# Performance work log

Hardware: AMD Instinct MI355X
Metric: run time of the kernel (lower is better)

## Reference

```python
import jax, jax.numpy as jnp
import numpy as np

N, E, C, K, M = 16384, 512, 128, 2048, 4
H1, H2 = 128, 256
EPS = 1e-5


def setup_inputs() -> dict:
    key = jax.random.key(0)
    ks = jax.random.split(key, 32)
    r = lambda k, shape, s=0.02: jax.random.normal(k, shape, dtype=jnp.float32) * s
    inp = {
        'x': jax.random.normal(ks[0], (N, E), dtype=jnp.float32),
        # per-book encoder params, stacked over M
        'enc_W1': r(ks[1], (M, E, H1)), 'enc_b1': r(ks[2], (M, H1)),
        'bn1_g': 1.0 + r(ks[3], (M, H1)), 'bn1_b': r(ks[4], (M, H1)),
        'bn1_m': r(ks[5], (M, H1), 0.1), 'bn1_v': jnp.ones((M, H1), jnp.float32),
        'enc_W2': r(ks[6], (M, H1, H2)), 'enc_b2': r(ks[7], (M, H2)),
        'bn2_g': 1.0 + r(ks[8], (M, H2)), 'bn2_b': r(ks[9], (M, H2)),
        'bn2_m': r(ks[10], (M, H2), 0.1), 'bn2_v': jnp.ones((M, H2), jnp.float32),
        'enc_W3': r(ks[11], (M, H2, C)), 'enc_b3': r(ks[12], (M, C)),
        # codebooks init uniform(-1/K, 1/K) as in torch source
        'codebooks': jax.random.uniform(ks[13], (M, K, C), jnp.float32, -1.0 / K, 1.0 / K),
        # decoder params
        'dec_W1': r(ks[14], (C, H2)), 'dec_b1': r(ks[15], (H2,)),
        'dbn1_g': 1.0 + r(ks[16], (H2,)), 'dbn1_b': r(ks[17], (H2,)),
        'dbn1_m': r(ks[18], (H2,), 0.1), 'dbn1_v': jnp.ones((H2,), jnp.float32),
        'dec_W2': r(ks[19], (H2, H1)), 'dec_b2': r(ks[20], (H1,)),
        'dbn2_g': 1.0 + r(ks[21], (H1,)), 'dbn2_b': r(ks[22], (H1,)),
        'dbn2_m': r(ks[23], (H1,), 0.1), 'dbn2_v': jnp.ones((H1,), jnp.float32),
        'dec_W3': r(ks[24], (H1, E)), 'dec_b3': r(ks[25], (E,)),
    }
    return inp


def _bn(h, g, b, m, v):
    # eval-mode BatchNorm1d with running stats (dropout inactive in eval)
    return (h - m) * (g / jnp.sqrt(v + EPS)) + b


def reference(x, enc_W1, enc_b1, bn1_g, bn1_b, bn1_m, bn1_v,
              enc_W2, enc_b2, bn2_g, bn2_b, bn2_m, bn2_v,
              enc_W3, enc_b3, codebooks,
              dec_W1, dec_b1, dbn1_g, dbn1_b, dbn1_m, dbn1_v,
              dec_W2, dec_b2, dbn2_g, dbn2_b, dbn2_m, dbn2_v,
              dec_W3, dec_b3):
    # encoders for all M books at once: [M, N, *]
    h = jnp.einsum('ne,mef->mnf', x, enc_W1) + enc_b1[:, None, :]
    h = jax.nn.relu(_bn(h, bn1_g[:, None], bn1_b[:, None], bn1_m[:, None], bn1_v[:, None]))
    h = jnp.einsum('mnf,mfg->mng', h, enc_W2) + enc_b2[:, None, :]
    h = jax.nn.relu(_bn(h, bn2_g[:, None], bn2_b[:, None], bn2_m[:, None], bn2_v[:, None]))
    ze = jnp.einsum('mng,mgc->mnc', h, enc_W3) + enc_b3[:, None, :]  # [M,N,C]

    # squared-distance VQ via dot-product expansion (same math as broadcast cdist)
    ze_sq = jnp.sum(ze * ze, axis=-1)                     # [M,N]
    cb_sq = jnp.sum(codebooks * codebooks, axis=-1)       # [M,K]
    cross = jnp.einsum('mnc,mkc->mnk', ze, codebooks)     # [M,N,K]
    dist = ze_sq[..., None] + cb_sq[:, None, :] - 2.0 * cross
    idx = jnp.argmin(dist, axis=-1)                       # [M,N]
    ce = jnp.take_along_axis(codebooks, idx[:, :, None], axis=1)  # [M,N,C]

    zq = jnp.sum(ce, axis=0)                              # [N,C]

    d = jnp.matmul(zq, dec_W1) + dec_b1
    d = jax.nn.relu(_bn(d, dbn1_g, dbn1_b, dbn1_m, dbn1_v))
    d = jnp.matmul(d, dec_W2) + dec_b2
    d = jax.nn.relu(_bn(d, dbn2_g, dbn2_b, dbn2_m, dbn2_v))
    x_hat = jnp.matmul(d, dec_W3) + dec_b3

    # res_list / ce_list returned as stacked [M,N,C] arrays
    return (x_hat, ze, ce)
```

## Files before the change

kernel.cpp:

```cpp
#include <hip/hip_runtime.h>
#include <hip/hip_bf16.h>
#include <stdint.h>

#define N_ROWS 16384
#define E_DIM 512
#define C_DIM 128
#define K_CODES 2048
#define M_BOOKS 4
#define H1_DIM 128
#define H2_DIM 256
#define EPS_V 1e-5f
#define VQ_RT 8

typedef __attribute__((ext_vector_type(8))) short short8v;
typedef __attribute__((ext_vector_type(4))) float f32x4;

#if defined(__has_builtin)
#if __has_builtin(__builtin_amdgcn_global_load_lds)
#define HAVE_GLL 1
#endif
#endif

#ifdef HAVE_GLL
__device__ __forceinline__ void gll16(const void* g, void* l) {
    __builtin_amdgcn_global_load_lds(
        (const __attribute__((address_space(1))) uint32_t*)g,
        (__attribute__((address_space(3))) uint32_t*)l, 16, 0, 0);
}
#endif

__device__ __forceinline__ unsigned int mapmono(float d) {
    unsigned int ub = __float_as_uint(d);
    return (ub & 0x80000000u) ? ~ub : (ub | 0x80000000u);
}
__device__ __forceinline__ float unmapmono(unsigned int u) {
    unsigned int bits = (u & 0x80000000u) ? (u & 0x7FFFFFFFu) : ~u;
    return __uint_as_float(bits);
}

template<int BK, bool BNRELU>
__global__ __launch_bounds__(256, 4) void gemm128(
    const float* __restrict__ A, const float* __restrict__ B,
    const float* __restrict__ bias, const float* __restrict__ bn_g,
    const float* __restrict__ bn_b, const float* __restrict__ bn_m,
    const float* __restrict__ bn_v, float* __restrict__ C,
    int Kd, int Hc, size_t sA, size_t sB, size_t sP, size_t sC)
{
    __shared__ float As[BK][128];
    __shared__ float Bs[BK][128];
    const int z = blockIdx.z;
    A += (size_t)z * sA; B += (size_t)z * sB; bias += (size_t)z * sP;
    if (BNRELU) {
        bn_g += (size_t)z * sP; bn_b += (size_t)z * sP;
        bn_m += (size_t)z * sP; bn_v += (size_t)z * sP;
    }
    const int t = threadIdx.x;
    const int tx = t & 15, ty = t >> 4;
    const int row0 = blockIdx.y * 128, col0 = blockIdx.x * 128;
    const int ar = t & 127, ak = (t >> 7) * 4;
    const int bc = (t & 31) * 4, bk0 = t >> 5;

    float acc[8][8] = {};
    for (int k0 = 0; k0 < Kd; k0 += BK) {
        #pragma unroll
        for (int l = 0; l < BK / 8; ++l) {
            const int lk = ak + l * 8;
            float4 av = *(const float4*)(A + (size_t)(row0 + ar) * Kd + (k0 + lk));
            As[lk+0][ar] = av.x; As[lk+1][ar] = av.y;
            As[lk+2][ar] = av.z; As[lk+3][ar] = av.w;
            const int kb = bk0 + l * 8;
            *(float4*)&Bs[kb][bc] =
                *(const float4*)(B + (size_t)(k0 + kb) * Hc + (col0 + bc));
        }
        __syncthreads();
        #pragma unroll
        for (int kk = 0; kk < BK; ++kk) {
            float a[8], b[8];
            *(float4*)&a[0] = *(const float4*)&As[kk][ty*4];
            *(float4*)&a[4] = *(const float4*)&As[kk][64 + ty*4];
            *(float4*)&b[0] = *(const float4*)&Bs[kk][tx*4];
            *(float4*)&b[4] = *(const float4*)&Bs[kk][64 + tx*4];
            #pragma unroll
            for (int i = 0; i < 8; ++i)
                #pragma unroll
                for (int j = 0; j < 8; ++j)
                    acc[i][j] = fmaf(a[i], b[j], acc[i][j]);
        }
        __syncthreads();
    }
    float bi[8], sc[8], mu[8], be[8];
    #pragma unroll
    for (int j = 0; j < 8; ++j) {
        const int col = col0 + ((j < 4) ? (tx*4 + j) : (64 + tx*4 + j - 4));
        bi[j] = bias[col];
        if (BNRELU) {
            sc[j] = bn_g[col] / sqrtf(bn_v[col] + EPS_V);
            mu[j] = bn_m[col]; be[j] = bn_b[col];
        }
    }
    #pragma unroll
    for (int i = 0; i < 8; ++i) {
        const int row = row0 + ((i < 4) ? (ty*4 + i) : (64 + ty*4 + i - 4));
        float v[8];
        #pragma unroll
        for (int j = 0; j < 8; ++j) {
            v[j] = acc[i][j] + bi[j];
            if (BNRELU) {
                float p = (v[j] - mu[j]) * sc[j];
                asm volatile("" : "+v"(p));
                v[j] = fmaxf(p + be[j], 0.0f);
            }
        }
        float* cp = C + (size_t)z * sC + (size_t)row * Hc + col0;
        *(float4*)(cp + tx*4)      = *(const float4*)&v[0];
        *(float4*)(cp + 64 + tx*4) = *(const float4*)&v[4];
    }
}

__global__ __launch_bounds__(256) void rowsq_np(const float* __restrict__ X,
                                                float* __restrict__ out, int rows)
{
    const int r = blockIdx.x * blockDim.x + threadIdx.x;
    if (r >= rows) return;
    const float* p = X + (size_t)r * C_DIM;
    float rr[8];
    #pragma unroll
    for (int j = 0; j < 8; ++j) {
        float v = p[j]; float s2 = v * v;
        asm volatile("" : "+v"(s2));
        rr[j] = s2;
    }
    for (int i = 8; i < C_DIM; i += 8) {
        #pragma unroll
        for (int j = 0; j < 8; ++j) {
            float v = p[i + j]; float s2 = v * v;
            asm volatile("" : "+v"(s2));
            rr[j] = rr[j] + s2;
        }
    }
    out[r] = ((rr[0]+rr[1]) + (rr[2]+rr[3])) + ((rr[4]+rr[5]) + (rr[6]+rr[7]));
}

__global__ __launch_bounds__(256) void split_ze(
    const float* __restrict__ ze, uint16_t* __restrict__ zeAf,
    float* __restrict__ zs, float* __restrict__ eps)
{
    const int m = blockIdx.y;
    const int r = blockIdx.x * 256 + threadIdx.x;
    const size_t g = (size_t)m * N_ROWS + r;
    const float* p = ze + g * C_DIM;
    float a[C_DIM];
    #pragma unroll
    for (int c4 = 0; c4 < C_DIM/4; ++c4) {
        float4 v = *(const float4*)(p + c4*4);
        a[c4*4+0]=v.x; a[c4*4+1]=v.y; a[c4*4+2]=v.z; a[c4*4+3]=v.w;
    }
    {
        float rr[8];
        #pragma unroll
        for (int j = 0; j < 8; ++j) {
            float v = a[j]; float s2 = v*v; asm volatile("" : "+v"(s2)); rr[j]=s2;
        }
        #pragma unroll
        for (int i = 8; i < C_DIM; i += 8)
            #pragma unroll
            for (int j = 0; j < 8; ++j) {
                float v = a[i+j]; float s2 = v*v; asm volatile("" : "+v"(s2));
                rr[j] = rr[j] + s2;
            }
        zs[g] = ((rr[0]+rr[1]) + (rr[2]+rr[3])) + ((rr[4]+rr[5]) + (rr[6]+rr[7]));
    }
    {
        float sab = 0.0f;
        #pragma unroll
        for (int c = 0; c < C_DIM; ++c) sab += fabsf(a[c]);
        eps[g] = sab * 4.8828125e-4f * 1e-4f + 1e-9f;
    }
    const int rt = r >> 7, rl = r & 127;
    uint16_t* base = zeAf + (size_t)m * 4194304 + ((size_t)rt * 4096 + rl) * 8;
    #pragma unroll
    for (int k8 = 0; k8 < 32; ++k8) {
        uint16_t u[8];
        #pragma unroll
        for (int j = 0; j < 8; ++j) {
            const int c = ((k8 < 16) ? k8 : (k8 - 16)) * 8 + j;
            __hip_bfloat16 h = __float2bfloat16(a[c]);
            if (k8 >= 16) {
                float res = a[c] - __bfloat162float(h);
                h = __float2bfloat16(res);
            }
            u[j] = *(uint16_t*)&h;
        }
        *(float4*)(base + (size_t)k8 * 1024) = *(const float4*)u;
    }
}

__global__ __launch_bounds__(256) void split_cb(
    const float* __restrict__ cb, uint16_t* __restrict__ cbBf,
    float* __restrict__ cbsq, int* __restrict__ count)
{
    const int m = blockIdx.z;
    const int k = blockIdx.x * 256 + threadIdx.x;
    if (m == 0 && k == 0) *count = 0;
    const float* p = cb + ((size_t)m * K_CODES + k) * C_DIM;
    float a[C_DIM];
    #pragma unroll
    for (int c4 = 0; c4 < C_DIM/4; ++c4) {
        float4 v = *(const float4*)(p + c4*4);
        a[c4*4+0]=v.x; a[c4*4+1]=v.y; a[c4*4+2]=v.z; a[c4*4+3]=v.w;
    }
    {
        float rr[8];
        #pragma unroll
        for (int j = 0; j < 8; ++j) {
            float v = a[j]; float s2 = v*v; asm volatile("" : "+v"(s2)); rr[j]=s2;
        }
        #pragma unroll
        for (int i = 8; i < C_DIM; i += 8)
            #pragma unroll
            for (int j = 0; j < 8; ++j) {
                float v = a[i+j]; float s2 = v*v; asm volatile("" : "+v"(s2));
                rr[j] = rr[j] + s2;
            }
        cbsq[(size_t)m * K_CODES + k] =
            ((rr[0]+rr[1]) + (rr[2]+rr[3])) + ((rr[4]+rr[5]) + (rr[6]+rr[7]));
    }
    const int ct = k >> 7, kl = k & 127;
    uint16_t* base = cbBf + (((size_t)m * 16 + ct) * 4096 + kl) * 8;
    #pragma unroll
    for (int k8 = 0; k8 < 32; ++k8) {
        uint16_t u[8];
        #pragma unroll
        for (int j = 0; j < 8; ++j) {
            const int c = ((k8 < 16) ? k8 : (k8 - 16)) * 8 + j;
            __hip_bfloat16 h = __float2bfloat16(a[c]);
            if (k8 >= 16) {
                float res = a[c] - __bfloat162float(h);
                h = __float2bfloat16(res);
            }
            u[j] = *(uint16_t*)&h;
        }
        *(float4*)(base + (size_t)k8 * 1024) = *(const float4*)u;
    }
}

__global__ __launch_bounds__(256, 2) void vq_mfma(
    const uint16_t* __restrict__ zeAf, const uint16_t* __restrict__ cbBf,
    const float* __restrict__ zs, const float* __restrict__ cbsq,
    unsigned long long* __restrict__ keysB, unsigned long long* __restrict__ keysS)
{
    __shared__ __align__(16) uint16_t Ball[32768];
    __shared__ unsigned long long kb2[128][2];

    const int t = threadIdx.x;
    const int l = t & 63, w = t >> 6;
    const int ct = blockIdx.y;
    const int rt0 = (blockIdx.x & 15) * VQ_RT;
    const int m = blockIdx.x >> 4;
    const int lq = l >> 4, lc = l & 15;

    const uint16_t* Bg = cbBf + ((size_t)m * 16 + ct) * 32768;
#ifdef HAVE_GLL
    #pragma unroll
    for (int i = 0; i < 16; ++i)
        gll16(Bg + (size_t)(t + i*256) * 8, Ball + (size_t)(t + i*256) * 8);
#else
    #pragma unroll
    for (int i = 0; i < 16; ++i)
        *(float4*)(Ball + (size_t)(t + i*256)*8) =
            *(const float4*)(Bg + (size_t)(t + i*256)*8);
#endif
    __syncthreads();

    const float* csb = cbsq + (size_t)m * K_CODES + ct*128;

    for (int ri = 0; ri < VQ_RT; ++ri) {
        const int rt = rt0 + ri;
        const uint16_t* Ag = zeAf + (size_t)m * 4194304 + (size_t)rt * 32768;
        f32x4 acc[2][8] = {};
        #pragma unroll
        for (int s = 0; s < 4; ++s) {
            short8v zeh[2], zel[2], cbf[8];
            #pragma unroll
            for (int rc = 0; rc < 2; ++rc) {
                const int row = w*32 + rc*16 + lc;
                zeh[rc] = *(const short8v*)(Ag + ((size_t)(s*4 + lq)*128 + row)*8);
                zel[rc] = *(const short8v*)(Ag + ((size_t)(16 + s*4 + lq)*128 + row)*8);
            }
            #pragma unroll
            for (int c8 = 0; c8 < 8; ++c8)
                cbf[c8] = *(const short8v*)(Ball + ((size_t)(s*4 + lq)*128 + c8*16 + lc)*8);
            #pragma unroll
            for (int rc = 0; rc < 2; ++rc)
                #pragma unroll
                for (int c8 = 0; c8 < 8; ++c8)
                    acc[rc][c8] = __builtin_amdgcn_mfma_f32_16x16x32_bf16(
                        cbf[c8], zeh[rc], acc[rc][c8], 0, 0, 0);
            #pragma unroll
            for (int rc = 0; rc < 2; ++rc)
                #pragma unroll
                for (int c8 = 0; c8 < 8; ++c8)
                    acc[rc][c8] = __builtin_amdgcn_mfma_f32_16x16x32_bf16(
                        cbf[c8], zel[rc], acc[rc][c8], 0, 0, 0);
            #pragma unroll
            for (int c8 = 0; c8 < 8; ++c8)
                cbf[c8] = *(const short8v*)(Ball + ((size_t)(16 + s*4 + lq)*128 + c8*16 + lc)*8);
            #pragma unroll
            for (int rc = 0; rc < 2; ++rc)
                #pragma unroll
                for (int c8 = 0; c8 < 8; ++c8)
                    acc[rc][c8] = __builtin_amdgcn_mfma_f32_16x16x32_bf16(
                        cbf[c8], zeh[rc], acc[rc][c8], 0, 0, 0);
        }

        #pragma unroll
        for (int rc = 0; rc < 2; ++rc) {
            const int row = w*32 + rc*16 + lc;
            float bd = 3.4e38f, sd = 3.4e38f;
            int bidx = 0;
            #pragma unroll
            for (int c8 = 0; c8 < 8; ++c8)
                #pragma unroll
                for (int q = 0; q < 4; ++q) {
                    const int cl = c8*16 + lq*4 + q;
                    const float d = fmaf(-2.0f, acc[rc][c8][q], csb[cl]);
                    const float mx = fmaxf(bd, d);
                    sd = fminf(sd, mx);
                    if (d < bd) { bd = d; bidx = ct*128 + cl; }
                }
            #pragma unroll
            for (int mk = 16; mk < 64; mk <<= 1) {
                const float ob = __shfl_xor(bd, mk);
                const int   oi = __shfl_xor(bidx, mk);
                const float os = __shfl_xor(sd, mk);
                const float mx = fmaxf(bd, ob);
                sd = fminf(fminf(sd, os), mx);
                if (ob < bd) { bd = ob; bidx = oi; }
            }
            if (lq == 0) {
                kb2[row][0] = ((unsigned long long)mapmono(bd) << 32) | (unsigned)bidx;
                kb2[row][1] = ((unsigned long long)mapmono(sd) << 32) | 0xFFFFFFFFu;
            }
        }
        __syncthreads();
        if (t < 128) {
            const unsigned long long b = kb2[t][0];
            const unsigned long long s2v = kb2[t][1];
            const size_t g = (size_t)m * N_ROWS + (size_t)rt*128 + t;
            const unsigned long long old = atomicMin(&keysB[g], b);
            const unsigned long long disp = (b < old) ? old : b;
            const unsigned long long cand = (s2v < disp) ? s2v : disp;
            atomicMin(&keysS[g], cand);
        }
        __syncthreads();
    }
}

__global__ __launch_bounds__(256) void vq_flag(
    const float* __restrict__ ze, const float* __restrict__ cb,
    const float* __restrict__ zs, const float* __restrict__ cbsq,
    unsigned long long* __restrict__ keysB,
    const unsigned long long* __restrict__ keysS,
    const float* __restrict__ eps, int* __restrict__ list, int* __restrict__ count)
{
    const int m = blockIdx.y;
    const int r = blockIdx.x * 256 + threadIdx.x;
    const size_t g = (size_t)m * N_ROWS + r;
    const unsigned long long kbv = keysB[g];
    const int code = (int)(kbv & 0xFFFFFFFFull);
    const float db = unmapmono((unsigned int)(kbv >> 32));
    const float ds2 = unmapmono((unsigned int)(keysS[g] >> 32));
    const float* zr = ze + g * C_DIM;
    const float* cr = cb + ((size_t)m * K_CODES + code) * C_DIM;
    float acc = 0.0f;
    #pragma unroll
    for (int c = 0; c < C_DIM; ++c) acc = fmaf(zr[c], cr[c], acc);
    const float dex = fmaf(-2.0f, acc, cbsq[(size_t)m * K_CODES + code]);
    const float e = eps[g];
    if ((ds2 - db <= 2.0f * e) || (fabsf(dex - db) > e)) {
        keysB[g] = ~0ull;
        const int p = atomicAdd(count, 1);
        list[p] = (int)g;
    }
}

__global__ __launch_bounds__(256) void vq_cleanup3(
    const float* __restrict__ ze, const float* __restrict__ cb,
    const float* __restrict__ zs, const float* __restrict__ cbsq,
    const int* __restrict__ list, const int* __restrict__ count,
    unsigned long long* __restrict__ keysB)
{
    __shared__ float zrow[C_DIM];
    __shared__ unsigned long long red[4];
    const int t = threadIdx.x;
    const int w = t >> 6, l = t & 63;
    const int ntot = (*count) * 8;
    for (int wi = blockIdx.x; wi < ntot; wi += gridDim.x) {
        const int idx = wi >> 3, ks = wi & 7;
        const int g = list[idx];
        const int m = g >> 14;
        __syncthreads();
        if (t < 32)
            *(float4*)(zrow + t*4) = *(const float4*)(ze + (size_t)g * C_DIM + t*4);
        __syncthreads();
        const float zsr = zs[g];
        const int code = ks * 256 + t;
        const float* cbp = cb + ((size_t)m * K_CODES + code) * C_DIM;
        float acc = 0.0f;
        #pragma unroll
        for (int c4 = 0; c4 < C_DIM/4; ++c4) {
            const float4 b4 = *(const float4*)(cbp + c4*4);
            acc = fmaf(zrow[c4*4+0], b4.x, acc);
            acc = fmaf(zrow[c4*4+1], b4.y, acc);
            acc = fmaf(zrow[c4*4+2], b4.z, acc);
            acc = fmaf(zrow[c4*4+3], b4.w, acc);
        }
        const float tmp = zsr + cbsq[(size_t)m * K_CODES + code];
        float m2a = 2.0f * acc;
        asm volatile("" : "+v"(m2a));
        const float d = tmp - m2a;
        unsigned long long key =
            ((unsigned long long)mapmono(d) << 32) | (unsigned)code;
        #pragma unroll
        for (int off2 = 32; off2 > 0; off2 >>= 1) {
            const unsigned long long o = __shfl_down(key, off2);
            key = (o < key) ? o : key;
        }
        if (l == 0) red[w] = key;
        __syncthreads();
        if (t == 0) {
            unsigned long long b = red[0];
            b = (red[1] < b) ? red[1] : b;
            b = (red[2] < b) ? red[2] : b;
            b = (red[3] < b) ? red[3] : b;
            atomicMin(&keysB[g], b);
        }
    }
}

__global__ __launch_bounds__(256) void split_wB(
    const float* __restrict__ W, uint16_t* __restrict__ Wf, int Kd, int Hc)
{
    const int z = blockIdx.z;
    W += (size_t)z * Kd * Hc;
    Wf += (size_t)z * Kd * Hc * 2;
    const int ct = blockIdx.x, k8 = blockIdx.y;
    const int Sh = Kd / 8, S = Kd / 4;
    const int t = threadIdx.x;
    #pragma unroll
    for (int e0 = 0; e0 < 2; ++e0) {
        const int e = t + e0 * 256;
        const int h = e >> 3, j = e & 7;
        const float v = W[(size_t)(k8*8 + j) * Hc + ct*64 + h];
        __hip_bfloat16 hi = __float2bfloat16(v);
        float res = v - __bfloat162float(hi);
        __hip_bfloat16 lo = __float2bfloat16(res);
        Wf[(((size_t)ct*S + k8)*64 + h)*8 + j]      = *(uint16_t*)&hi;
        Wf[(((size_t)ct*S + Sh + k8)*64 + h)*8 + j] = *(uint16_t*)&lo;
    }
}

template<bool BNRELU>
__global__ __launch_bounds__(256, 3) void mfma_fused(
    const float* __restrict__ A, const uint16_t* __restrict__ Wf,
    const float* __restrict__ bias, const float* __restrict__ bn_g,
    const float* __restrict__ bn_b, const float* __restrict__ bn_m,
    const float* __restrict__ bn_v, float* __restrict__ C, int Kd, int Hc,
    size_t sA, size_t sWf, size_t sP, size_t sC)
{
    __shared__ __align__(16) uint16_t Ah[4096], Al[4096], Bh[2048], Bl[2048];
    const int z = blockIdx.z;
    A += (size_t)z * sA; Wf += (size_t)z * sWf; bias += (size_t)z * sP;
    if (BNRELU) {
        bn_g += (size_t)z * sP; bn_b += (size_t)z * sP;
        bn_m += (size_t)z * sP; bn_v += (size_t)z * sP;
    }
    C += (size_t)z * sC;

    const int t = threadIdx.x;
    const int l = t & 63, w = t >> 6;
    const int kq = l >> 4, lc = l & 15;
    const int row0 = blockIdx.y * 128, col0 = blockIdx.x * 64;
    const int Sh = Kd / 8, S = Kd / 4;
    const uint16_t* Wct = Wf + (size_t)blockIdx.x * S * 512;

    f32x4 acc[2][4] = {};
    const int arow = t & 127, khalf = t >> 7;
    for (int ks = 0; ks < Kd / 32; ++ks) {
        const float* ap = A + (size_t)(row0 + arow) * Kd + ks*32 + khalf*16;
        float fa[16];
        *(float4*)&fa[0]  = *(const float4*)(ap);
        *(float4*)&fa[4]  = *(const float4*)(ap + 4);
        *(float4*)&fa[8]  = *(const float4*)(ap + 8);
        *(float4*)&fa[12] = *(const float4*)(ap + 12);
        uint16_t ah[16], al16[16];
        #pragma unroll
        for (int i = 0; i < 16; ++i) {
            __hip_bfloat16 h = __float2bfloat16(fa[i]);
            float res = fa[i] - __bfloat162float(h);
            __hip_bfloat16 lo = __float2bfloat16(res);
            ah[i] = *(uint16_t*)&h; al16[i] = *(uint16_t*)&lo;
        }
        #pragma unroll
        for (int kql = 0; kql < 2; ++kql) {
            const int kq_ = khalf*2 + kql;
            *(float4*)(Ah + ((size_t)kq_*128 + arow)*8) = *(const float4*)&ah[kql*8];
            *(float4*)(Al + ((size_t)kq_*128 + arow)*8) = *(const float4*)&al16[kql*8];
        }
        {
            const int sec = t >> 6, off = (t & 63) * 8;
            *(float4*)(Bh + (size_t)sec*512 + off) =
                *(const float4*)(Wct + ((size_t)(ks*4 + sec))*512 + off);
            *(float4*)(Bl + (size_t)sec*512 + off) =
                *(const float4*)(Wct + ((size_t)(Sh + ks*4 + sec))*512 + off);
        }
        __syncthreads();
        short8v afh[2], afl[2], bfh[4], bfl[4];
        #pragma unroll
        for (int r2 = 0; r2 < 2; ++r2) {
            afh[r2] = *(const short8v*)(Ah + ((size_t)kq*128 + w*32 + r2*16 + lc)*8);
            afl[r2] = *(const short8v*)(Al + ((size_t)kq*128 + w*32 + r2*16 + lc)*8);
        }
        #pragma unroll
        for (int c4 = 0; c4 < 4; ++c4) {
            bfh[c4] = *(const short8v*)(Bh + ((size_t)kq*64 + c4*16 + lc)*8);
            bfl[c4] = *(const short8v*)(Bl + ((size_t)kq*64 + c4*16 + lc)*8);
        }
        #pragma unroll
        for (int r2 = 0; r2 < 2; ++r2)
            #pragma unroll
            for (int c4 = 0; c4 < 4; ++c4) {
                acc[r2][c4] = __builtin_amdgcn_mfma_f32_16x16x32_bf16(
                    afh[r2], bfh[c4], acc[r2][c4], 0, 0, 0);
                acc[r2][c4] = __builtin_amdgcn_mfma_f32_16x16x32_bf16(
                    afl[r2], bfh[c4], acc[r2][c4], 0, 0, 0);
                acc[r2][c4] = __builtin_amdgcn_mfma_f32_16x16x32_bf16(
                    afh[r2], bfl[c4], acc[r2][c4], 0, 0, 0);
            }
        __syncthreads();
    }
    #pragma unroll
    for (int c4 = 0; c4 < 4; ++c4) {
        const int col = col0 + c4*16 + lc;
        const float bi = bias[col];
        float sc = 0.f, mu = 0.f, be = 0.f;
        if (BNRELU) {
            sc = bn_g[col] / sqrtf(bn_v[col] + EPS_V);
            mu = bn_m[col]; be = bn_b[col];
        }
        #pragma unroll
        for (int r2 = 0; r2 < 2; ++r2)
            #pragma unroll
            for (int q = 0; q < 4; ++q) {
                const int row = row0 + w*32 + r2*16 + kq*4 + q;
                float v = acc[r2][c4][q] + bi;
                if (BNRELU) v = fmaxf((v - mu) * sc + be, 0.0f);
                C[(size_t)row * Hc + col] = v;
            }
    }
}

__global__ __launch_bounds__(256, 4) void vq_argmin(
    const float* __restrict__ ze, const float* __restrict__ cb,
    const float* __restrict__ ze_sq, const float* __restrict__ cb_sq,
    unsigned long long* __restrict__ keys)
{
    __shared__ __align__(16) char smem_raw[32768];
    float* As = (float*)smem_raw;
    float* Bs = As + 32*128;
    unsigned long long* kb = (unsigned long long*)smem_raw;
    const int m = blockIdx.z;
    const float* Zm  = ze + (size_t)m * N_ROWS * C_DIM;
    const float* Bm  = cb + (size_t)m * K_CODES * C_DIM;
    const float* zsm = ze_sq + (size_t)m * N_ROWS;
    const float* csm = cb_sq + (size_t)m * K_CODES;
    const int t = threadIdx.x;
    const int tx = t & 15, ty = t >> 4;
    const int row0 = blockIdx.y * 128, col0 = blockIdx.x * 128;
    const int ar = t & 127, ak = (t >> 7) * 4;
    float acc[8][8] = {};
    for (int k0 = 0; k0 < C_DIM; k0 += 32) {
        #pragma unroll
        for (int l = 0; l < 4; ++l) {
            const int lk = ak + l * 8;
            float4 av = *(const float4*)(Zm + (size_t)(row0 + ar) * C_DIM + (k0 + lk));
            As[(lk+0)*128+ar] = av.x; As[(lk+1)*128+ar] = av.y;
            As[(lk+2)*128+ar] = av.z; As[(lk+3)*128+ar] = av.w;
            float4 bv = *(const float4*)(Bm + (size_t)(col0 + ar) * C_DIM + (k0 + lk));
            Bs[(lk+0)*128+ar] = bv.x; Bs[(lk+1)*128+ar] = bv.y;
            Bs[(lk+2)*128+ar] = bv.z; Bs[(lk+3)*128+ar] = bv.w;
        }
        __syncthreads();
        #pragma unroll
        for (int kk = 0; kk < 32; ++kk) {
            float a[8], b[8];
            *(float4*)&a[0] = *(const float4*)&As[kk*128 + ty*4];
            *(float4*)&a[4] = *(const float4*)&As[kk*128 + 64 + ty*4];
            *(float4*)&b[0] = *(const float4*)&Bs[kk*128 + tx*4];
            *(float4*)&b[4] = *(const float4*)&Bs[kk*128 + 64 + tx*4];
            #pragma unroll
            for (int i = 0; i < 8; ++i)
                #pragma unroll
                for (int j = 0; j < 8; ++j)
                    acc[i][j] = fmaf(a[i], b[j], acc[i][j]);
        }
        __syncthreads();
    }
    unsigned long long mykey[8];
    #pragma unroll
    for (int i = 0; i < 8; ++i) {
        const int rloc = (i < 4) ? (ty*4 + i) : (64 + ty*4 + i - 4);
        const float zsv = zsm[row0 + rloc];
        unsigned long long bk = ~0ull;
        #pragma unroll
        for (int j = 0; j < 8; ++j) {
            const int code = col0 + ((j < 4) ? (tx*4 + j) : (64 + tx*4 + j - 4));
            const float d = (zsv + csm[code]) - 2.0f * acc[i][j];
            const unsigned long long key =
                ((unsigned long long)mapmono(d) << 32) | (unsigned)code;
            bk = (key < bk) ? key : bk;
        }
        mykey[i] = bk;
    }
    __syncthreads();
    #pragma unroll
    for (int i = 0; i < 8; ++i) {
        const int rloc = (i < 4) ? (ty*4 + i) : (64 + ty*4 + i - 4);
        kb[rloc*17 + tx] = mykey[i];
    }
    __syncthreads();
    if (t < 128) {
        unsigned long long bk = kb[t*17];
        #pragma unroll
        for (int k2 = 1; k2 < 16; ++k2) {
            const unsigned long long k = kb[t*17 + k2];
            bk = (k < bk) ? k : bk;
        }
        atomicMin(&keys[(size_t)m * N_ROWS + row0 + t], bk);
    }
}

__global__ __launch_bounds__(256) void gather_ce_zq(
    const unsigned long long* __restrict__ keys, const float* __restrict__ cb,
    float* __restrict__ ce_out, float* __restrict__ zq)
{
    const int gid = blockIdx.x * 256 + threadIdx.x;
    const int n = gid >> 7, c = gid & 127;
    float s = 0.0f;
    #pragma unroll
    for (int m = 0; m < M_BOOKS; ++m) {
        const int idx = (int)(keys[(size_t)m * N_ROWS + n] & 0xFFFFFFFFull);
        const float v = cb[((size_t)m * K_CODES + idx) * C_DIM + c];
        ce_out[((size_t)m * N_ROWS + n) * (size_t)C_DIM + c] = v;
        s += v;
    }
    zq[gid] = s;
}

extern "C" void kernel_launch(void* const* d_in, const int* in_sizes, int n_in,
                              void* d_out, int out_size, void* d_ws, size_t ws_size,
                              hipStream_t stream)
{
    const float* x   = (const float*)d_in[0];
    const float* eW1 = (const float*)d_in[1];
    const float* eb1 = (const float*)d_in[2];
    const float* g1  = (const float*)d_in[3];
    const float* b1  = (const float*)d_in[4];
    const float* m1  = (const float*)d_in[5];
    const float* v1  = (const float*)d_in[6];
    const float* eW2 = (const float*)d_in[7];
    const float* eb2 = (const float*)d_in[8];
    const float* g2  = (const float*)d_in[9];
    const float* b2  = (const float*)d_in[10];
    const float* m2  = (const float*)d_in[11];
    const float* v2  = (const float*)d_in[12];
    const float* eW3 = (const float*)d_in[13];
    const float* eb3 = (const float*)d_in[14];
    const float* cb  = (const float*)d_in[15];
    const float* dW1 = (const float*)d_in[16];
    const float* db1 = (const float*)d_in[17];
    const float* dg1 = (const float*)d_in[18];
    const float* dbb1= (const float*)d_in[19];
    const float* dm1 = (const float*)d_in[20];
    const float* dv1 = (const float*)d_in[21];
    const float* dW2 = (const float*)d_in[22];
    const float* db2 = (const float*)d_in[23];
    const float* dg2 = (const float*)d_in[24];
    const float* dbb2= (const float*)d_in[25];
    const float* dm2 = (const float*)d_in[26];
    const float* dv2 = (const float*)d_in[27];
    const float* dW3 = (const float*)d_in[28];
    const float* db3 = (const float*)d_in[29];

    float* out_xhat = (float*)d_out;
    float* out_ze   = out_xhat + (size_t)N_ROWS * E_DIM;
    float* out_ce   = out_ze + (size_t)M_BOOKS * N_ROWS * C_DIM;

    float* ws = (float*)d_ws;
    const size_t h1N1 = (size_t)N_ROWS * H1_DIM;
    const size_t h2N1 = (size_t)N_ROWS * H2_DIM;

    const size_t vqNeedF = 8192 + 65536 + 65536 + 8388608 + 1048576
                         + 131072 + 131072 + 65536 + 16
                         + 32768 + 32768 + 65536
                         + 524288 + 131072 + 131072;
    const bool tierA = ws_size >= ((size_t)M_BOOKS*(h1N1+h2N1) + vqNeedF + 64) * 4;
    const bool tierB = ws_size >= ((h1N1+h2N1) + vqNeedF + 64) * 4;

    dim3 blk(256, 1, 1);

    if (tierB) {
        size_t off = 0;
        float* h1 = ws; off += (tierA ? M_BOOKS : 1) * h1N1;
        float* h2 = ws + off; off += (tierA ? M_BOOKS : 1) * h2N1;
        float* cbsq = ws + off; off += 8192;
        float* zsb = ws + off; off += 65536;
        float* epsb = ws + off; off += 65536;
        uint16_t* zeAf = (uint16_t*)(ws + off); off += 8388608;
        uint16_t* cbBf = (uint16_t*)(ws + off); off += 1048576;
        unsigned long long* keysB = (unsigned long long*)(ws + off); off += 131072;
        unsigned long long* keysS = (unsigned long long*)(ws + off); off += 131072;
        int* list = (int*)(ws + off); off += 65536;
        int* count = (int*)(ws + off); off += 16;
        uint16_t* w1f = (uint16_t*)(ws + off); off += 32768;
        uint16_t* w2f = (uint16_t*)(ws + off); off += 32768;
        uint16_t* w3f = (uint16_t*)(ws + off); off += 65536;
        uint16_t* we1f = (uint16_t*)(ws + off); off += 524288;
        uint16_t* we2f = (uint16_t*)(ws + off); off += 131072;
        uint16_t* we3f = (uint16_t*)(ws + off); off += 131072;
        float* zq = h1; float* d1 = h2; float* d2 = h1;

        split_cb<<<dim3(K_CODES/256, 1, M_BOOKS), blk, 0, stream>>>(cb, cbBf, cbsq, count);
        split_wB<<<dim3(H1_DIM/64, E_DIM/8, M_BOOKS), blk, 0, stream>>>(eW1, we1f, E_DIM, H1_DIM);
        split_wB<<<dim3(H2_DIM/64, H1_DIM/8, M_BOOKS), blk, 0, stream>>>(eW2, we2f, H1_DIM, H2_DIM);
        split_wB<<<dim3(C_DIM/64, H2_DIM/8, M_BOOKS), blk, 0, stream>>>(eW3, we3f, H2_DIM, C_DIM);
        split_wB<<<dim3(H2_DIM/64, C_DIM/8, 1), blk, 0, stream>>>(dW1, w1f, C_DIM, H2_DIM);
        split_wB<<<dim3(H1_DIM/64, H2_DIM/8, 1), blk, 0, stream>>>(dW2, w2f, H2_DIM, H1_DIM);
        split_wB<<<dim3(E_DIM/64, H1_DIM/8, 1), blk, 0, stream>>>(dW3, w3f, H1_DIM, E_DIM);
        hipMemsetAsync((void*)keysB, 0xFF, (size_t)M_BOOKS * N_ROWS * 8 * 2, stream);

        const int nz = tierA ? M_BOOKS : 1;
        const int nloop = tierA ? 1 : M_BOOKS;
        for (int p = 0; p < nloop; ++p) {
            const size_t mb = tierA ? 0 : (size_t)p;
            mfma_fused<true><<<dim3(H1_DIM/64, N_ROWS/128, nz), blk, 0, stream>>>(
                x, we1f + mb*(size_t)E_DIM*H1_DIM*2,
                eb1 + mb*H1_DIM, g1 + mb*H1_DIM, b1 + mb*H1_DIM, m1 + mb*H1_DIM, v1 + mb*H1_DIM,
                h1, E_DIM, H1_DIM,
                0, (size_t)E_DIM*H1_DIM*2, H1_DIM, h1N1);
            mfma_fused<true><<<dim3(H2_DIM/64, N_ROWS/128, nz), blk, 0, stream>>>(
                h1, we2f + mb*(size_t)H1_DIM*H2_DIM*2,
                eb2 + mb*H2_DIM, g2 + mb*H2_DIM, b2 + mb*H2_DIM, m2 + mb*H2_DIM, v2 + mb*H2_DIM,
                h2, H1_DIM, H2_DIM,
                h1N1, (size_t)H1_DIM*H2_DIM*2, H2_DIM, h2N1);
            mfma_fused<false><<<dim3(C_DIM/64, N_ROWS/128, nz), blk, 0, stream>>>(
                h2, we3f + mb*(size_t)H2_DIM*C_DIM*2,
                eb3 + mb*C_DIM, nullptr, nullptr, nullptr, nullptr,
                out_ze + mb*(size_t)N_ROWS*C_DIM, H2_DIM, C_DIM,
                h2N1, (size_t)H2_DIM*C_DIM*2, C_DIM, (size_t)N_ROWS*C_DIM);
        }

        split_ze<<<dim3(N_ROWS/256, M_BOOKS), blk, 0, stream>>>(out_ze, zeAf, zsb, epsb);
        vq_mfma<<<dim3(16 * M_BOOKS, K_CODES/128, 1), blk, 0, stream>>>(
            zeAf, cbBf, zsb, cbsq, keysB, keysS);
        vq_flag<<<dim3(N_ROWS/256, M_BOOKS), blk, 0, stream>>>(
            out_ze, cb, zsb, cbsq, keysB, keysS, epsb, list, count);
        vq_cleanup3<<<dim3(2048), blk, 0, stream>>>(
            out_ze, cb, zsb, cbsq, list, count, keysB);

        gather_ce_zq<<<dim3((N_ROWS*C_DIM)/256), blk, 0, stream>>>(keysB, cb, out_ce, zq);
        mfma_fused<true><<<dim3(H2_DIM/64, N_ROWS/128, 1), blk, 0, stream>>>(
            zq, w1f, db1, dg1, dbb1, dm1, dv1, d1, C_DIM, H2_DIM, 0, 0, 0, 0);
        mfma_fused<true><<<dim3(H1_DIM/64, N_ROWS/128, 1), blk, 0, stream>>>(
            d1, w2f, db2, dg2, dbb2, dm2, dv2, d2, H2_DIM, H1_DIM, 0, 0, 0, 0);
        mfma_fused<false><<<dim3(E_DIM/64, N_ROWS/128, 1), blk, 0, stream>>>(
            d2, w3f, db3, nullptr, nullptr, nullptr, nullptr,
            out_xhat, H1_DIM, E_DIM, 0, 0, 0, 0);
        return;
    }

    {
        const size_t smallN = (size_t)M_BOOKS*N_ROWS + (size_t)M_BOOKS*K_CODES
                            + 2 + 2*(size_t)M_BOOKS*N_ROWS;
        const size_t fullFloats = (size_t)M_BOOKS*(h1N1 + h2N1) + smallN;
        const bool fM = ws_size >= fullFloats * sizeof(float) + 256;
        size_t off = 0;
        float* h1 = ws; off += (fM ? M_BOOKS : 1) * h1N1;
        float* h2 = ws + off; off += (fM ? M_BOOKS : 1) * h2N1;
        float* zesq = ws + off; off += (size_t)M_BOOKS * N_ROWS;
        float* cbsq = ws + off; off += (size_t)M_BOOKS * K_CODES;
        off = (off + 1) & ~(size_t)1;
        unsigned long long* keys = (unsigned long long*)(ws + off);
        float* zq = h1; float* d1 = h2; float* d2 = h1;
        hipMemsetAsync((void*)keys, 0xFF, (size_t)M_BOOKS * N_ROWS * 8, stream);
        const int nz = fM ? M_BOOKS : 1;
        const int nloop = fM ? 1 : M_BOOKS;
        for (int p = 0; p < nloop; ++p) {
            const size_t mb = fM ? 0 : (size_t)p;
            gemm128<32, true><<<dim3(H1_DIM/128, N_ROWS/128, nz), blk, 0, stream>>>(
                x, eW1 + mb*(size_t)E_DIM*H1_DIM,
                eb1 + mb*H1_DIM, g1 + mb*H1_DIM, b1 + mb*H1_DIM, m1 + mb*H1_DIM, v1 + mb*H1_DIM,
                h1, E_DIM, H1_DIM, 0, (size_t)E_DIM*H1_DIM, H1_DIM, h1N1);
            gemm128<32, true><<<dim3(H2_DIM/128, N_ROWS/128, nz), blk, 0, stream>>>(
                h1, eW2 + mb*(size_t)H1_DIM*H2_DIM,
                eb2 + mb*H2_DIM, g2 + mb*H2_DIM, b2 + mb*H2_DIM, m2 + mb*H2_DIM, v2 + mb*H2_DIM,
                h2, H1_DIM, H2_DIM, h1N1, (size_t)H1_DIM*H2_DIM, H2_DIM, h2N1);
            gemm128<32, false><<<dim3(C_DIM/128, N_ROWS/128, nz), blk, 0, stream>>>(
                h2, eW3 + mb*(size_t)H2_DIM*C_DIM,
                eb3 + mb*C_DIM, nullptr, nullptr, nullptr, nullptr,
                out_ze + mb*(size_t)N_ROWS*C_DIM, H2_DIM, C_DIM,
                h2N1, (size_t)H2_DIM*C_DIM, C_DIM, (size_t)N_ROWS*C_DIM);
        }
        rowsq_np<<<dim3((M_BOOKS*N_ROWS)/256), blk, 0, stream>>>(out_ze, zesq, M_BOOKS*N_ROWS);
        rowsq_np<<<dim3((M_BOOKS*K_CODES)/256), blk, 0, stream>>>(cb, cbsq, M_BOOKS*K_CODES);
        vq_argmin<<<dim3(K_CODES/128, N_ROWS/128, M_BOOKS), blk, 0, stream>>>(
            out_ze, cb, zesq, cbsq, keys);
        gather_ce_zq<<<dim3((N_ROWS*C_DIM)/256), blk, 0, stream>>>(keys, cb, out_ce, zq);
        gemm128<32, true><<<dim3(H2_DIM/128, N_ROWS/128, 1), blk, 0, stream>>>(
            zq, dW1, db1, dg1, dbb1, dm1, dv1, d1, C_DIM, H2_DIM, 0, 0, 0, 0);
        gemm128<32, true><<<dim3(H1_DIM/128, N_ROWS/128, 1), blk, 0, stream>>>(
            d1, dW2, db2, dg2, dbb2, dm2, dv2, d2, H2_DIM, H1_DIM, 0, 0, 0, 0);
        gemm128<32, false><<<dim3(E_DIM/128, N_ROWS/128, 1), blk, 0, stream>>>(
            d2, dW3, db3, nullptr, nullptr, nullptr, nullptr,
            out_xhat, H1_DIM, E_DIM, 0, 0, 0, 0);
    }
}
```

Measured before the change: 358.1 us.

## Pre-split x into bf16 hi/lo tiles, add setprio around MFMA, simplify VQ flag

```diff
diff --git a/kernel.cpp b/kernel.cpp
--- a/kernel.cpp
+++ b/kernel.cpp
@@ -141,6 +141,31 @@
     out[r] = ((rr[0]+rr[1]) + (rr[2]+rr[3])) + ((rr[4]+rr[5]) + (rr[6]+rr[7]));
 }
 
+__global__ __launch_bounds__(256) void split_x(
+    const float* __restrict__ x, uint16_t* __restrict__ xf)
+{
+    const int r = blockIdx.x * 256 + threadIdx.x;
+    const int rt = r >> 7, rl = r & 127;
+    const float* p = x + (size_t)r * E_DIM;
+    uint16_t* base = xf + (size_t)rt * (E_DIM * 256) + (size_t)rl * 8;
+    #pragma unroll 4
+    for (int k8 = 0; k8 < E_DIM / 8; ++k8) {
+        float a[8];
+        *(float4*)&a[0] = *(const float4*)(p + k8*8);
+        *(float4*)&a[4] = *(const float4*)(p + k8*8 + 4);
+        uint16_t uh[8], ul[8];
+        #pragma unroll
+        for (int j = 0; j < 8; ++j) {
+            __hip_bfloat16 h = __float2bfloat16(a[j]);
+            float res = a[j] - __bfloat162float(h);
+            __hip_bfloat16 lo = __float2bfloat16(res);
+            uh[j] = *(uint16_t*)&h; ul[j] = *(uint16_t*)&lo;
+        }
+        *(float4*)(base + (size_t)k8 * 1024) = *(const float4*)uh;
+        *(float4*)(base + (size_t)(E_DIM/8 + k8) * 1024) = *(const float4*)ul;
+    }
+}
+
 __global__ __launch_bounds__(256) void split_ze(
     const float* __restrict__ ze, uint16_t* __restrict__ zeAf,
     float* __restrict__ zs, float* __restrict__ eps)
@@ -290,6 +315,7 @@
             #pragma unroll
             for (int c8 = 0; c8 < 8; ++c8)
                 cbf[c8] = *(const short8v*)(Ball + ((size_t)(s*4 + lq)*128 + c8*16 + lc)*8);
+            __builtin_amdgcn_s_setprio(1);
             #pragma unroll
             for (int rc = 0; rc < 2; ++rc)
                 #pragma unroll
@@ -302,15 +328,18 @@
                 for (int c8 = 0; c8 < 8; ++c8)
                     acc[rc][c8] = __builtin_amdgcn_mfma_f32_16x16x32_bf16(
                         cbf[c8], zel[rc], acc[rc][c8], 0, 0, 0);
+            __builtin_amdgcn_s_setprio(0);
             #pragma unroll
             for (int c8 = 0; c8 < 8; ++c8)
                 cbf[c8] = *(const short8v*)(Ball + ((size_t)(16 + s*4 + lq)*128 + c8*16 + lc)*8);
+            __builtin_amdgcn_s_setprio(1);
             #pragma unroll
             for (int rc = 0; rc < 2; ++rc)
                 #pragma unroll
                 for (int c8 = 0; c8 < 8; ++c8)
                     acc[rc][c8] = __builtin_amdgcn_mfma_f32_16x16x32_bf16(
                         cbf[c8], zeh[rc], acc[rc][c8], 0, 0, 0);
+            __builtin_amdgcn_s_setprio(0);
         }
 
         #pragma unroll
@@ -357,8 +386,6 @@
 }
 
 __global__ __launch_bounds__(256) void vq_flag(
-    const float* __restrict__ ze, const float* __restrict__ cb,
-    const float* __restrict__ zs, const float* __restrict__ cbsq,
     unsigned long long* __restrict__ keysB,
     const unsigned long long* __restrict__ keysS,
     const float* __restrict__ eps, int* __restrict__ list, int* __restrict__ count)
@@ -366,18 +393,9 @@
     const int m = blockIdx.y;
     const int r = blockIdx.x * 256 + threadIdx.x;
     const size_t g = (size_t)m * N_ROWS + r;
-    const unsigned long long kbv = keysB[g];
-    const int code = (int)(kbv & 0xFFFFFFFFull);
-    const float db = unmapmono((unsigned int)(kbv >> 32));
+    const float db = unmapmono((unsigned int)(keysB[g] >> 32));
     const float ds2 = unmapmono((unsigned int)(keysS[g] >> 32));
-    const float* zr = ze + g * C_DIM;
-    const float* cr = cb + ((size_t)m * K_CODES + code) * C_DIM;
-    float acc = 0.0f;
-    #pragma unroll
-    for (int c = 0; c < C_DIM; ++c) acc = fmaf(zr[c], cr[c], acc);
-    const float dex = fmaf(-2.0f, acc, cbsq[(size_t)m * K_CODES + code]);
-    const float e = eps[g];
-    if ((ds2 - db <= 2.0f * e) || (fabsf(dex - db) > e)) {
+    if (ds2 - db <= 2.0f * eps[g]) {
         keysB[g] = ~0ull;
         const int p = atomicAdd(count, 1);
         list[p] = (int)g;
@@ -520,6 +538,87 @@
         for (int r2 = 0; r2 < 2; ++r2) {
             afh[r2] = *(const short8v*)(Ah + ((size_t)kq*128 + w*32 + r2*16 + lc)*8);
             afl[r2] = *(const short8v*)(Al + ((size_t)kq*128 + w*32 + r2*16 + lc)*8);
+        }
+        #pragma unroll
+        for (int c4 = 0; c4 < 4; ++c4) {
+            bfh[c4] = *(const short8v*)(Bh + ((size_t)kq*64 + c4*16 + lc)*8);
+            bfl[c4] = *(const short8v*)(Bl + ((size_t)kq*64 + c4*16 + lc)*8);
+        }
+        #pragma unroll
+        for (int r2 = 0; r2 < 2; ++r2)
+            #pragma unroll
+            for (int c4 = 0; c4 < 4; ++c4) {
+                acc[r2][c4] = __builtin_amdgcn_mfma_f32_16x16x32_bf16(
+                    afh[r2], bfh[c4], acc[r2][c4], 0, 0, 0);
+                acc[r2][c4] = __builtin_amdgcn_mfma_f32_16x16x32_bf16(
+                    afl[r2], bfh[c4], acc[r2][c4], 0, 0, 0);
+                acc[r2][c4] = __builtin_amdgcn_mfma_f32_16x16x32_bf16(
+                    afh[r2], bfl[c4], acc[r2][c4], 0, 0, 0);
+            }
+        __syncthreads();
+    }
+    #pragma unroll
+    for (int c4 = 0; c4 < 4; ++c4) {
+        const int col = col0 + c4*16 + lc;
+        const float bi = bias[col];
+        float sc = 0.f, mu = 0.f, be = 0.f;
+        if (BNRELU) {
+            sc = bn_g[col] / sqrtf(bn_v[col] + EPS_V);
+            mu = bn_m[col]; be = bn_b[col];
+        }
+        #pragma unroll
+        for (int r2 = 0; r2 < 2; ++r2)
+            #pragma unroll
+            for (int q = 0; q < 4; ++q) {
+                const int row = row0 + w*32 + r2*16 + kq*4 + q;
+                float v = acc[r2][c4][q] + bi;
+                if (BNRELU) v = fmaxf((v - mu) * sc + be, 0.0f);
+                C[(size_t)row * Hc + col] = v;
+            }
+    }
+}
+
+template<bool BNRELU>
+__global__ __launch_bounds__(256, 3) void mfma_fusedA(
+    const uint16_t* __restrict__ Af, const uint16_t* __restrict__ Wf,
+    const float* __restrict__ bias, const float* __restrict__ bn_g,
+    const float* __restrict__ bn_b, const float* __restrict__ bn_m,
+    const float* __restrict__ bn_v, float* __restrict__ C, int Kd, int Hc,
+    size_t sWf, size_t sP, size_t sC)
+{
+    __shared__ __align__(16) uint16_t Bh[2048], Bl[2048];
+    const int z = blockIdx.z;
+    Wf += (size_t)z * sWf; bias += (size_t)z * sP;
+    if (BNRELU) {
+        bn_g += (size_t)z * sP; bn_b += (size_t)z * sP;
+        bn_m += (size_t)z * sP; bn_v += (size_t)z * sP;
+    }
+    C += (size_t)z * sC;
+
+    const int t = threadIdx.x;
+    const int l = t & 63, w = t >> 6;
+    const int kq = l >> 4, lc = l & 15;
+    const int row0 = blockIdx.y * 128, col0 = blockIdx.x * 64;
+    const int Sh = Kd / 8, S = Kd / 4;
+    const uint16_t* Wct = Wf + (size_t)blockIdx.x * S * 512;
+    const uint16_t* Ag = Af + (size_t)blockIdx.y * (size_t)Kd * 256;
+
+    f32x4 acc[2][4] = {};
+    for (int ks = 0; ks < Kd / 32; ++ks) {
+        {
+            const int sec = t >> 6, off = (t & 63) * 8;
+            *(float4*)(Bh + (size_t)sec*512 + off) =
+                *(const float4*)(Wct + ((size_t)(ks*4 + sec))*512 + off);
+            *(float4*)(Bl + (size_t)sec*512 + off) =
+                *(const float4*)(Wct + ((size_t)(Sh + ks*4 + sec))*512 + off);
+        }
+        __syncthreads();
+        short8v afh[2], afl[2], bfh[4], bfl[4];
+        #pragma unroll
+        for (int r2 = 0; r2 < 2; ++r2) {
+            const int row = w*32 + r2*16 + lc;
+            afh[r2] = *(const short8v*)(Ag + ((size_t)(ks*4 + kq)*128 + row)*8);
+            afl[r2] = *(const short8v*)(Ag + ((size_t)(Sh + ks*4 + kq)*128 + row)*8);
         }
         #pragma unroll
         for (int c4 = 0; c4 < 4; ++c4) {
@@ -730,6 +829,7 @@
         uint16_t* we3f = (uint16_t*)(ws + off); off += 131072;
         float* zq = h1; float* d1 = h2; float* d2 = h1;
 
+        split_x<<<dim3(N_ROWS/256), blk, 0, stream>>>(x, zeAf);
         split_cb<<<dim3(K_CODES/256, 1, M_BOOKS), blk, 0, stream>>>(cb, cbBf, cbsq, count);
         split_wB<<<dim3(H1_DIM/64, E_DIM/8, M_BOOKS), blk, 0, stream>>>(eW1, we1f, E_DIM, H1_DIM);
         split_wB<<<dim3(H2_DIM/64, H1_DIM/8, M_BOOKS), blk, 0, stream>>>(eW2, we2f, H1_DIM, H2_DIM);
@@ -743,11 +843,11 @@
         const int nloop = tierA ? 1 : M_BOOKS;
         for (int p = 0; p < nloop; ++p) {
             const size_t mb = tierA ? 0 : (size_t)p;
-            mfma_fused<true><<<dim3(H1_DIM/64, N_ROWS/128, nz), blk, 0, stream>>>(
-                x, we1f + mb*(size_t)E_DIM*H1_DIM*2,
+            mfma_fusedA<true><<<dim3(H1_DIM/64, N_ROWS/128, nz), blk, 0, stream>>>(
+                zeAf, we1f + mb*(size_t)E_DIM*H1_DIM*2,
                 eb1 + mb*H1_DIM, g1 + mb*H1_DIM, b1 + mb*H1_DIM, m1 + mb*H1_DIM, v1 + mb*H1_DIM,
                 h1, E_DIM, H1_DIM,
-                0, (size_t)E_DIM*H1_DIM*2, H1_DIM, h1N1);
+                (size_t)E_DIM*H1_DIM*2, H1_DIM, h1N1);
             mfma_fused<true><<<dim3(H2_DIM/64, N_ROWS/128, nz), blk, 0, stream>>>(
                 h1, we2f + mb*(size_t)H1_DIM*H2_DIM*2,
                 eb2 + mb*H2_DIM, g2 + mb*H2_DIM, b2 + mb*H2_DIM, m2 + mb*H2_DIM, v2 + mb*H2_DIM,
@@ -764,7 +864,7 @@
         vq_mfma<<<dim3(16 * M_BOOKS, K_CODES/128, 1), blk, 0, stream>>>(
             zeAf, cbBf, zsb, cbsq, keysB, keysS);
         vq_flag<<<dim3(N_ROWS/256, M_BOOKS), blk, 0, stream>>>(
-            out_ze, cb, zsb, cbsq, keysB, keysS, epsb, list, count);
+            keysB, keysS, epsb, list, count);
         vq_cleanup3<<<dim3(2048), blk, 0, stream>>>(
             out_ze, cb, zsb, cbsq, list, count, keysB);
 
```

Result: slower. 365.5 us (+2.1%).
